# Optimization experiments

Measured on AMD Instinct MI355X. Metric: run time of the kernel, lower is better.

## Reference

```python
import jax, jax.numpy as jnp
import numpy as np

N = 100000
E = 1600000
IN_C, HID_C, OUT_C = 64, 64, 40
EPS = 1e-5


def setup_inputs() -> dict:
    key = jax.random.key(0)
    ks = jax.random.split(key, 16)
    x = jax.random.normal(ks[0], (N, IN_C), dtype=jnp.float32)
    edge_index = jax.random.randint(ks[1], (2, E), 0, N, dtype=jnp.int64)

    def glorot(k, fan_in, fan_out):
        s = jnp.sqrt(6.0 / (fan_in + fan_out)).astype(jnp.float32)
        return jax.random.uniform(k, (fan_in, fan_out), jnp.float32, -s, s)

    return {
        "x": x,
        "edge_index": edge_index,
        # layer 0: SAGEConv(IN_C -> HID_C): out = mean_aggr @ Wl + x @ Wr + b
        "Wl0": glorot(ks[2], IN_C, HID_C), "Wr0": glorot(ks[3], IN_C, HID_C),
        "b0": jnp.zeros((HID_C,), jnp.float32),
        # layer 1: SAGEConv(HID_C -> HID_C)
        "Wl1": glorot(ks[4], HID_C, HID_C), "Wr1": glorot(ks[5], HID_C, HID_C),
        "b1": jnp.zeros((HID_C,), jnp.float32),
        # layer 2: SAGEConv(HID_C -> OUT_C)
        "Wl2": glorot(ks[6], HID_C, OUT_C), "Wr2": glorot(ks[7], HID_C, OUT_C),
        "b2": jnp.zeros((OUT_C,), jnp.float32),
        # batch norms after layers 0 and 1
        "g0": jnp.ones((HID_C,), jnp.float32), "be0": jnp.zeros((HID_C,), jnp.float32),
        "g1": jnp.ones((HID_C,), jnp.float32), "be1": jnp.zeros((HID_C,), jnp.float32),
    }


def _sage_conv(x, src, dst, Wl, Wr, b):
    # mean aggregation of source features at destination nodes (PyG SAGEConv, aggr='mean')
    agg = jax.ops.segment_sum(x[src], dst, num_segments=N)  # [N, C]
    deg = jax.ops.segment_sum(jnp.ones((src.shape[0],), x.dtype), dst, num_segments=N)
    mean = agg / jnp.maximum(deg, 1.0)[:, None]
    return mean @ Wl + x @ Wr + b


def _batch_norm(x, gamma, beta):
    mu = jnp.mean(x, axis=0)
    var = jnp.var(x, axis=0)
    return (x - mu) * jax.lax.rsqrt(var + EPS) * gamma + beta


def reference(x, edge_index, Wl0, Wr0, b0, Wl1, Wr1, b1, Wl2, Wr2, b2, g0, be0, g1, be1):
    src, dst = edge_index[0], edge_index[1]
    h = _sage_conv(x, src, dst, Wl0, Wr0, b0)
    h = jax.nn.relu(_batch_norm(h, g0, be0))  # dropout is identity at inference
    h = _sage_conv(h, src, dst, Wl1, Wr1, b1)
    h = jax.nn.relu(_batch_norm(h, g1, be1))
    return _sage_conv(h, src, dst, Wl2, Wr2, b2)
```

## Files before the change

kernel.cpp:

```cpp
#include <hip/hip_runtime.h>


constexpr float BN_EPS = 1e-5f;

typedef __attribute__((ext_vector_type(8))) short bf16x8;
typedef __attribute__((ext_vector_type(4))) float f32x4;

__device__ __forceinline__ float bf2f(unsigned short u) {
  union { unsigned int i; float f; } c;
  c.i = (unsigned int)u << 16;
  return c.f;
}
__device__ __forceinline__ unsigned short f2bf(float v) {
  union { float f; unsigned int i; } c;
  c.f = v;
  unsigned int r = c.i + 0x7fffu + ((c.i >> 16) & 1u);
  return (unsigned short)(r >> 16);
}

__device__ __forceinline__ void st_f(float* p, size_t i, float v) { p[i] = v; }
__device__ __forceinline__ void st_f(unsigned short* p, size_t i, float v) {
  p[i] = f2bf(v);
}

__device__ __forceinline__ float4 ld_row(const float* p, int row, int li) {
  return ((const float4*)p)[(size_t)row * 16 + li];
}
__device__ __forceinline__ float4 ld_row(const unsigned short* p, int row, int li) {
  ushort4 u = ((const ushort4*)p)[(size_t)row * 16 + li];
  float4 f;
  f.x = bf2f(u.x); f.y = bf2f(u.y); f.z = bf2f(u.z); f.w = bf2f(u.w);
  return f;
}

__global__ __launch_bounds__(256) void k_probe(const int* __restrict__ w, int E,
                                               int* __restrict__ dflag) {
  __shared__ int any;
  if (threadIdx.x == 0) any = 0;
  __syncthreads();
  const int twoE = 2 * E;
  int local = 0;
  for (int i = 0; i < 8; ++i) {
    long long idx = (long long)(threadIdx.x * 8 + i) * twoE / 2048;
    int wi = (int)(idx | 1);
    if (wi < twoE && w[wi] != 0) local = 1;
  }
  if (local) atomicOr(&any, 1);
  __syncthreads();
  if (threadIdx.x == 0) *dflag = any;
}

__device__ __forceinline__ void load_edge(const void* ei, int e, int E, int is32,
                                          int& src, int& dst) {
  if (is32) {
    const int* p = (const int*)ei;
    src = p[e];
    dst = p[E + e];
  } else {
    const long long* p = (const long long*)ei;
    src = (int)p[e];
    dst = (int)p[(long long)E + e];
  }
}

__global__ __launch_bounds__(256) void k_hist(const void* __restrict__ ei, int E,
                                              int N, const int* __restrict__ dflag,
                                              int NB, int chunk,
                                              int* __restrict__ hist) {
  __shared__ int h[256];
  h[threadIdx.x] = 0;
  __syncthreads();
  const int is32 = *dflag;
  int lo = blockIdx.x * chunk;
  int hi = lo + chunk;
  if (hi > E) hi = E;
  for (int e = lo + threadIdx.x; e < hi; e += 256) {
    int src, dst;
    load_edge(ei, e, E, is32, src, dst);
    if ((unsigned)src < (unsigned)N && (unsigned)dst < (unsigned)N)
      atomicAdd(&h[dst >> 9], 1);
  }
  __syncthreads();
  if (threadIdx.x < NB) hist[blockIdx.x * NB + threadIdx.x] = h[threadIdx.x];
}

__global__ __launch_bounds__(256) void k_btot(const int* __restrict__ hist,
                                              int NBLK, int NB,
                                              int* __restrict__ bucket_base,
                                              float* __restrict__ stats) {
  stats[threadIdx.x] = 0.0f;
  __shared__ int part[256];
  int t = threadIdx.x;
  int s = 0;
  if (t < NB)
    for (int b = 0; b < NBLK; ++b) s += hist[b * NB + t];
  part[t] = s;
  __syncthreads();
  for (int off = 1; off < 256; off <<= 1) {
    int u = (t >= off) ? part[t - off] : 0;
    __syncthreads();
    part[t] += u;
    __syncthreads();
  }
  if (t < NB) bucket_base[t] = part[t] - s;
  if (t == NB - 1) bucket_base[NB] = part[t];
}

__global__ __launch_bounds__(64) void k_hoff(const int* __restrict__ hist,
                                             int NBLK, int NB,
                                             const int* __restrict__ bucket_base,
                                             int* __restrict__ offs) {
  int b = blockIdx.x;
  int lane = threadIdx.x;
  int carry = bucket_base[b];
  for (int c = 0; c < NBLK; c += 64) {
    int blk = c + lane;
    int v = (blk < NBLK) ? hist[blk * NB + b] : 0;
    int incl = v;
    for (int off = 1; off < 64; off <<= 1) {
      int u = __shfl_up(incl, off);
      if (lane >= off) incl += u;
    }
    if (blk < NBLK) offs[blk * NB + b] = carry + incl - v;
    carry += __shfl(incl, 63);
  }
}

__global__ __launch_bounds__(256) void k_scat(const void* __restrict__ ei, int E,
                                              int N, const int* __restrict__ dflag,
                                              int NB, int chunk,
                                              const int* __restrict__ offs,
                                              unsigned* __restrict__ csr) {
  __shared__ int cur[256];
  if (threadIdx.x < NB) cur[threadIdx.x] = offs[blockIdx.x * NB + threadIdx.x];
  __syncthreads();
  const int is32 = *dflag;
  int lo = blockIdx.x * chunk;
  int hi = lo + chunk;
  if (hi > E) hi = E;
  for (int e = lo + threadIdx.x; e < hi; e += 256) {
    int src, dst;
    load_edge(ei, e, E, is32, src, dst);
    if ((unsigned)src < (unsigned)N && (unsigned)dst < (unsigned)N) {
      int p = atomicAdd(&cur[dst >> 9], 1);
      csr[p] = ((unsigned)src << 9) | (unsigned)(dst & 511);
    }
  }
}

__global__ __launch_bounds__(256) void k_fine(unsigned* __restrict__ csr,
                                              const int* __restrict__ bucket_base,
                                              int N, int* __restrict__ row_start) {
  constexpr int CAP = 12288;
  __shared__ unsigned lrec[CAP];
  __shared__ int lcnt[512];
  __shared__ int cur[512];
  __shared__ int wtot[4];
  const int b = blockIdx.x;
  const int lo = bucket_base[b];
  int cnt = bucket_base[b + 1] - lo;
  if (cnt > CAP) cnt = CAP;
  const int t = threadIdx.x;
  lcnt[t] = 0;
  lcnt[t + 256] = 0;
  __syncthreads();
  for (int i = t; i < cnt; i += 256) {
    unsigned r = csr[lo + i];
    lrec[i] = r;
    atomicAdd(&lcnt[r & 511], 1);
  }
  __syncthreads();
  int v0 = lcnt[2 * t], v1 = lcnt[2 * t + 1];
  int s = v0 + v1;
  int incl = s;
  const int lane = t & 63;
  for (int off = 1; off < 64; off <<= 1) {
    int u = __shfl_up(incl, off);
    if (lane >= off) incl += u;
  }
  const int wv = t >> 6;
  if (lane == 63) wtot[wv] = incl;
  __syncthreads();
  int woff = 0;
  for (int i = 0; i < wv; ++i) woff += wtot[i];
  int excl = woff + incl - s;
  cur[2 * t] = excl;
  cur[2 * t + 1] = excl + v0;
  int gi = b * 512 + 2 * t;
  if (gi <= N) row_start[gi] = lo + excl;
  if (gi + 1 <= N) row_start[gi + 1] = lo + excl + v0;
  __syncthreads();
  for (int i = t; i < cnt; i += 256) {
    unsigned r = lrec[i];
    int p = atomicAdd(&cur[r & 511], 1);
    csr[lo + p] = r >> 9;
  }
}

template <int COUT, bool BNIN, bool BNOUT, typename TI, typename TO>
__global__ __launch_bounds__(256, 4) void k_sage(
    const TI* __restrict__ hin, const int* __restrict__ row_start,
    const int* __restrict__ csr, const float* __restrict__ Wl,
    const float* __restrict__ Wr, const float* __restrict__ bias,
    const float* __restrict__ statsIn, const float* __restrict__ gIn,
    const float* __restrict__ beIn, float* __restrict__ statsOut,
    TO* __restrict__ out, int n) {
  constexpr int NT = (COUT + 15) / 16;
  __shared__ short sWf[NT][4][64][8];
  __shared__ short sA[4][16][136];
  __shared__ float sBN[2][64];
  __shared__ float sRed[2][4][64];

  for (int t = threadIdx.x; t < NT * 4 * 64; t += 256) {
    int lane = t & 63;
    int kt = (t >> 6) & 3;
    int nt = t >> 8;
    int kbase = kt * 32 + (lane >> 4) * 8;
    int col = nt * 16 + (lane & 15);
#pragma unroll
    for (int j = 0; j < 8; ++j) {
      int k = kbase + j;
      float wv = 0.0f;
      if (col < COUT) wv = (k < 64) ? Wl[k * COUT + col] : Wr[(k - 64) * COUT + col];
      sWf[nt][kt][lane][j] = (short)f2bf(wv);
    }
  }
  if (BNIN && threadIdx.x < 64) {
    int c = threadIdx.x;
    float inv = 1.0f / (float)n;
    float mu = statsIn[c] * inv;
    float var = statsIn[64 + c] * inv - mu * mu;
    var = var < 0.f ? 0.f : var;
    float sc = gIn[c] * rsqrtf(var + BN_EPS);
    sBN[0][c] = sc;
    sBN[1][c] = beIn[c] - mu * sc;
  }
  __syncthreads();

  const int wave = threadIdx.x >> 6;
  const int lane = threadIdx.x & 63;
  const int g = lane >> 4;
  const int li = lane & 15;
  const int quad = lane >> 4;
  const int col16 = lane & 15;

  float4 bsc = make_float4(1.f, 1.f, 1.f, 1.f);
  float4 bsh = make_float4(0.f, 0.f, 0.f, 0.f);
  if (BNIN) {
    bsc = *(const float4*)&sBN[0][li * 4];
    bsh = *(const float4*)&sBN[1][li * 4];
  }
  auto xf = [&](float4 v) -> float4 {
    if (!BNIN) return v;
    float4 r;
    r.x = fmaxf(v.x * bsc.x + bsh.x, 0.f);
    r.y = fmaxf(v.y * bsc.y + bsh.y, 0.f);
    r.z = fmaxf(v.z * bsc.z + bsh.z, 0.f);
    r.w = fmaxf(v.w * bsc.w + bsh.w, 0.f);
    return r;
  };

  float bias_r[NT];
#pragma unroll
  for (int nt = 0; nt < NT; ++nt) {
    int c = nt * 16 + col16;
    bias_r[nt] = (c < COUT) ? bias[c] : 0.0f;
  }

  float statS[NT], statQ[NT];
#pragma unroll
  for (int nt = 0; nt < NT; ++nt) { statS[nt] = 0.f; statQ[nt] = 0.f; }

  const int wgl = blockIdx.x * 4 + wave;
  const int nstride = gridDim.x * 64;

  for (int base = wgl * 16; base < n; base += nstride) {
#pragma unroll 1
    for (int nb = 0; nb < 16; ++nb) {
      int node = base + nb;
      if (node >= n) break;
      int rs = row_start[node];
      int re = row_start[node + 1];
      float4 acc = make_float4(0.f, 0.f, 0.f, 0.f);
      int e = rs + g;
      for (; e + 12 < re; e += 16) {
        int r0 = csr[e], r1 = csr[e + 4], r2 = csr[e + 8], r3 = csr[e + 12];
        float4 a = xf(ld_row(hin, r0, li));
        float4 b = xf(ld_row(hin, r1, li));
        float4 c = xf(ld_row(hin, r2, li));
        float4 d = xf(ld_row(hin, r3, li));
        acc.x += (a.x + b.x) + (c.x + d.x);
        acc.y += (a.y + b.y) + (c.y + d.y);
        acc.z += (a.z + b.z) + (c.z + d.z);
        acc.w += (a.w + b.w) + (c.w + d.w);
      }
      for (; e < re; e += 4) {
        float4 a = xf(ld_row(hin, csr[e], li));
        acc.x += a.x; acc.y += a.y; acc.z += a.z; acc.w += a.w;
      }
      acc.x += __shfl_xor(acc.x, 16); acc.x += __shfl_xor(acc.x, 32);
      acc.y += __shfl_xor(acc.y, 16); acc.y += __shfl_xor(acc.y, 32);
      acc.z += __shfl_xor(acc.z, 16); acc.z += __shfl_xor(acc.z, 32);
      acc.w += __shfl_xor(acc.w, 16); acc.w += __shfl_xor(acc.w, 32);
      int deg = re - rs;
      float invd = 1.0f / (float)(deg > 0 ? deg : 1);
      float4 self = xf(ld_row(hin, node, li));
      ushort4 mv, sv;
      mv.x = f2bf(acc.x * invd); mv.y = f2bf(acc.y * invd);
      mv.z = f2bf(acc.z * invd); mv.w = f2bf(acc.w * invd);
      sv.x = f2bf(self.x); sv.y = f2bf(self.y);
      sv.z = f2bf(self.z); sv.w = f2bf(self.w);
      *(ushort4*)&sA[wave][nb][li * 4] = mv;
      *(ushort4*)&sA[wave][nb][64 + li * 4] = sv;
    }
    __builtin_amdgcn_wave_barrier();

    f32x4 acc[NT];
#pragma unroll
    for (int nt = 0; nt < NT; ++nt) acc[nt] = (f32x4){0.f, 0.f, 0.f, 0.f};
#pragma unroll
    for (int kt = 0; kt < 4; ++kt) {
      bf16x8 a = *(const bf16x8*)&sA[wave][lane & 15][kt * 32 + (lane >> 4) * 8];
#pragma unroll
      for (int nt = 0; nt < NT; ++nt) {
        bf16x8 b = *(const bf16x8*)&sWf[nt][kt][lane][0];
        acc[nt] = __builtin_amdgcn_mfma_f32_16x16x32_bf16(a, b, acc[nt], 0, 0, 0);
      }
    }
    __builtin_amdgcn_wave_barrier();

#pragma unroll
    for (int nt = 0; nt < NT; ++nt) {
      int c = nt * 16 + col16;
      if (c < COUT) {
#pragma unroll
        for (int r = 0; r < 4; ++r) {
          int node = base + quad * 4 + r;
          if (node < n) {
            float v = acc[nt][r] + bias_r[nt];
            st_f(out, (size_t)node * COUT + c, v);
            if (BNOUT) { statS[nt] += v; statQ[nt] += v * v; }
          }
        }
      }
    }
  }

  if (BNOUT) {
#pragma unroll
    for (int nt = 0; nt < NT; ++nt) {
      statS[nt] += __shfl_xor(statS[nt], 16);
      statS[nt] += __shfl_xor(statS[nt], 32);
      statQ[nt] += __shfl_xor(statQ[nt], 16);
      statQ[nt] += __shfl_xor(statQ[nt], 32);
    }
    if (quad == 0) {
#pragma unroll
      for (int nt = 0; nt < NT; ++nt) {
        sRed[0][wave][nt * 16 + col16] = statS[nt];
        sRed[1][wave][nt * 16 + col16] = statQ[nt];
      }
    }
    __syncthreads();
    if (threadIdx.x < 64) {
      int c = threadIdx.x;
      float s = sRed[0][0][c] + sRed[0][1][c] + sRed[0][2][c] + sRed[0][3][c];
      float q = sRed[1][0][c] + sRed[1][1][c] + sRed[1][2][c] + sRed[1][3][c];
      atomicAdd(&statsOut[c], s);
      atomicAdd(&statsOut[64 + c], q);
    }
  }
}

extern "C" void kernel_launch(void* const* d_in, const int* in_sizes, int n_in,
                              void* d_out, int out_size, void* d_ws, size_t ws_size,
                              hipStream_t stream) {
  const float* x = (const float*)d_in[0];
  const void* ei = d_in[1];
  const float* Wl0 = (const float*)d_in[2];
  const float* Wr0 = (const float*)d_in[3];
  const float* b0 = (const float*)d_in[4];
  const float* Wl1 = (const float*)d_in[5];
  const float* Wr1 = (const float*)d_in[6];
  const float* b1 = (const float*)d_in[7];
  const float* Wl2 = (const float*)d_in[8];
  const float* Wr2 = (const float*)d_in[9];
  const float* b2 = (const float*)d_in[10];
  const float* g0 = (const float*)d_in[11];
  const float* be0 = (const float*)d_in[12];
  const float* g1 = (const float*)d_in[13];
  const float* be1 = (const float*)d_in[14];

  const int N = in_sizes[0] / 64;
  const int E = in_sizes[1] / 2;
  const int NB = (N + 511) >> 9;
  const int NBLK = 256;
  const int chunk = (E + NBLK - 1) / NBLK;

  char* w = (char*)d_ws;
  auto carve = [&](size_t bytes) {
    void* p = (void*)w;
    w += (bytes + 255) & ~(size_t)255;
    return p;
  };
  int* dflag = (int*)carve(4);
  float* stats = (float*)carve(1024);
  int* row_start = (int*)carve((size_t)(N + 1) * 4);
  unsigned* csr = (unsigned*)carve((size_t)E * 4);
  int* hist = (int*)carve((size_t)NBLK * NB * 4);
  int* offs = (int*)carve((size_t)NBLK * NB * 4);
  int* bucket_base = (int*)carve((size_t)(NB + 1) * 4);

  float* statsA = stats;
  float* statsB = stats + 128;

  unsigned short* B = (unsigned short*)d_out;
  unsigned short* A = (unsigned short*)const_cast<float*>(x);

  const int SG = 1024;

  k_probe<<<1, 256, 0, stream>>>((const int*)ei, E, dflag);
  k_hist<<<NBLK, 256, 0, stream>>>(ei, E, N, dflag, NB, chunk, hist);
  k_btot<<<1, 256, 0, stream>>>(hist, NBLK, NB, bucket_base, stats);
  k_hoff<<<NB, 64, 0, stream>>>(hist, NBLK, NB, bucket_base, offs);
  k_scat<<<NBLK, 256, 0, stream>>>(ei, E, N, dflag, NB, chunk, offs, csr);
  k_fine<<<NB, 256, 0, stream>>>(csr, bucket_base, N, row_start);

  k_sage<64, false, true, float, unsigned short><<<SG, 256, 0, stream>>>(
      x, row_start, (const int*)csr, Wl0, Wr0, b0,
      statsA, g0, be0, statsA, B, N);

  k_sage<64, true, true, unsigned short, unsigned short><<<SG, 256, 0, stream>>>(
      B, row_start, (const int*)csr, Wl1, Wr1, b1,
      statsA, g0, be0, statsB, A, N);

  k_sage<40, true, false, unsigned short, float><<<SG, 256, 0, stream>>>(
      A, row_start, (const int*)csr, Wl2, Wr2, b2,
      statsB, g1, be1, statsB, (float*)d_out, N);
}
```

Before: 516.4 us.

## Gather neighbor features from FP8 copies in layers 1 and 2

Adds conversion kernels that turn the bf16 hidden activations into packed FP8 (e4m3) copies. Layers 1 and 2 then gather neighbour rows from these copies, halving the bytes per random row read in the dominant aggregation loop, while self rows stay in bf16. It also folds the per-bucket offset scan into the bucket-total kernel, removing one launch. The cost is two extra conversion passes and an FP8 quantisation error in the mean aggregation that may break accuracy tolerance.

```diff
diff --git a/kernel.cpp b/kernel.cpp
--- a/kernel.cpp
+++ b/kernel.cpp
@@ -5,6 +5,7 @@
 
 typedef __attribute__((ext_vector_type(8))) short bf16x8;
 typedef __attribute__((ext_vector_type(4))) float f32x4;
+typedef __attribute__((ext_vector_type(2))) float f32x2;
 
 __device__ __forceinline__ float bf2f(unsigned short u) {
   union { unsigned int i; float f; } c;
@@ -23,6 +24,68 @@
   p[i] = f2bf(v);
 }
 
+#if __has_builtin(__builtin_amdgcn_cvt_pk_f32_fp8) && \
+    __has_builtin(__builtin_amdgcn_cvt_pk_fp8_f32)
+#define HW_FP8 1
+#endif
+
+__device__ __forceinline__ float4 dec8(unsigned v) {
+#ifdef HW_FP8
+  f32x2 lo = __builtin_amdgcn_cvt_pk_f32_fp8((int)v, false);
+  f32x2 hi = __builtin_amdgcn_cvt_pk_f32_fp8((int)v, true);
+  float4 r;
+  r.x = lo[0]; r.y = lo[1]; r.z = hi[0]; r.w = hi[1];
+  return r;
+#else
+  auto d1 = [](unsigned b) -> float {
+    unsigned s = (b & 0x80u) << 24;
+    unsigned e = (b >> 3) & 15u, m = b & 7u;
+    unsigned bits;
+    if (e) bits = s | ((e + 120u) << 23) | (m << 20);
+    else if (m) {
+      int sh = (m & 4u) ? 0 : ((m & 2u) ? 1 : 2);
+      bits = s | ((114u - sh) << 23) | ((m << (sh + 21)) & 0x7FFFFFu);
+    } else
+      bits = s;
+    union { unsigned u; float f; } c;
+    c.u = bits;
+    return c.f;
+  };
+  float4 r;
+  r.x = d1(v & 255u); r.y = d1((v >> 8) & 255u);
+  r.z = d1((v >> 16) & 255u); r.w = d1(v >> 24);
+  return r;
+#endif
+}
+
+__device__ __forceinline__ unsigned enc8(float4 f) {
+#ifdef HW_FP8
+  int p = 0;
+  p = __builtin_amdgcn_cvt_pk_fp8_f32(f.x, f.y, p, false);
+  p = __builtin_amdgcn_cvt_pk_fp8_f32(f.z, f.w, p, true);
+  return (unsigned)p;
+#else
+  auto e1 = [](float x) -> unsigned {
+    union { float f; unsigned u; } c;
+    c.f = x;
+    unsigned s = (c.u >> 24) & 0x80u;
+    float a = fabsf(x);
+    if (a >= 464.f) return s | 0x7Eu;
+    if (a < 0.0009765625f) {
+      unsigned m = (unsigned)rintf(a * 512.f);
+      return s | (m & 7u);
+    }
+    c.f = a;
+    unsigned r = c.u + 0x7FFFFu + ((c.u >> 20) & 1u);
+    unsigned e = (r >> 23) - 120u;
+    unsigned m = (r >> 20) & 7u;
+    if (e >= 16u || (e == 15u && m == 7u)) return s | 0x7Eu;
+    return s | (e << 3) | m;
+  };
+  return e1(f.x) | (e1(f.y) << 8) | (e1(f.z) << 16) | (e1(f.w) << 24);
+#endif
+}
+
 __device__ __forceinline__ float4 ld_row(const float* p, int row, int li) {
   return ((const float4*)p)[(size_t)row * 16 + li];
 }
@@ -31,6 +94,9 @@
   float4 f;
   f.x = bf2f(u.x); f.y = bf2f(u.y); f.z = bf2f(u.z); f.w = bf2f(u.w);
   return f;
+}
+__device__ __forceinline__ float4 ld_row8(const unsigned* p, int row, int li) {
+  return dec8(p[(size_t)row * 16 + li]);
 }
 
 __global__ __launch_bounds__(256) void k_probe(const int* __restrict__ w, int E,
@@ -87,6 +153,7 @@
 __global__ __launch_bounds__(256) void k_btot(const int* __restrict__ hist,
                                               int NBLK, int NB,
                                               int* __restrict__ bucket_base,
+                                              int* __restrict__ offs,
                                               float* __restrict__ stats) {
   stats[threadIdx.x] = 0.0f;
   __shared__ int part[256];
@@ -104,25 +171,13 @@
   }
   if (t < NB) bucket_base[t] = part[t] - s;
   if (t == NB - 1) bucket_base[NB] = part[t];
-}
-
-__global__ __launch_bounds__(64) void k_hoff(const int* __restrict__ hist,
-                                             int NBLK, int NB,
-                                             const int* __restrict__ bucket_base,
-                                             int* __restrict__ offs) {
-  int b = blockIdx.x;
-  int lane = threadIdx.x;
-  int carry = bucket_base[b];
-  for (int c = 0; c < NBLK; c += 64) {
-    int blk = c + lane;
-    int v = (blk < NBLK) ? hist[blk * NB + b] : 0;
-    int incl = v;
-    for (int off = 1; off < 64; off <<= 1) {
-      int u = __shfl_up(incl, off);
-      if (lane >= off) incl += u;
-    }
-    if (blk < NBLK) offs[blk * NB + b] = carry + incl - v;
-    carry += __shfl(incl, 63);
+  __syncthreads();
+  if (t < NB) {
+    int carry = bucket_base[t];
+    for (int b = 0; b < NBLK; ++b) {
+      offs[b * NB + t] = carry;
+      carry += hist[b * NB + t];
+    }
   }
 }
 
@@ -197,14 +252,24 @@
   }
 }
 
-template <int COUT, bool BNIN, bool BNOUT, typename TI, typename TO>
+__global__ __launch_bounds__(256) void k_cvt8(const unsigned short* __restrict__ src,
+                                              unsigned* __restrict__ dst, int n16) {
+  int i = blockIdx.x * 256 + threadIdx.x;
+  if (i >= n16) return;
+  ushort4 u = ((const ushort4*)src)[i];
+  float4 f;
+  f.x = bf2f(u.x); f.y = bf2f(u.y); f.z = bf2f(u.z); f.w = bf2f(u.w);
+  dst[i] = enc8(f);
+}
+
+template <int COUT, bool BNIN, bool BNOUT, bool FP8, typename TI, typename TO>
 __global__ __launch_bounds__(256, 4) void k_sage(
-    const TI* __restrict__ hin, const int* __restrict__ row_start,
-    const int* __restrict__ csr, const float* __restrict__ Wl,
-    const float* __restrict__ Wr, const float* __restrict__ bias,
-    const float* __restrict__ statsIn, const float* __restrict__ gIn,
-    const float* __restrict__ beIn, float* __restrict__ statsOut,
-    TO* __restrict__ out, int n) {
+    const TI* __restrict__ hin, const unsigned* __restrict__ hin8,
+    const int* __restrict__ row_start, const int* __restrict__ csr,
+    const float* __restrict__ Wl, const float* __restrict__ Wr,
+    const float* __restrict__ bias, const float* __restrict__ statsIn,
+    const float* __restrict__ gIn, const float* __restrict__ beIn,
+    float* __restrict__ statsOut, TO* __restrict__ out, int n) {
   constexpr int NT = (COUT + 15) / 16;
   __shared__ short sWf[NT][4][64][8];
   __shared__ short sA[4][16][136];
@@ -258,6 +323,10 @@
     r.z = fmaxf(v.z * bsc.z + bsh.z, 0.f);
     r.w = fmaxf(v.w * bsc.w + bsh.w, 0.f);
     return r;
+  };
+  auto mrow = [&](int row) -> float4 {
+    if (FP8) return ld_row8(hin8, row, li);
+    return ld_row(hin, row, li);
   };
 
   float bias_r[NT];
@@ -285,17 +354,17 @@
       int e = rs + g;
       for (; e + 12 < re; e += 16) {
         int r0 = csr[e], r1 = csr[e + 4], r2 = csr[e + 8], r3 = csr[e + 12];
-        float4 a = xf(ld_row(hin, r0, li));
-        float4 b = xf(ld_row(hin, r1, li));
-        float4 c = xf(ld_row(hin, r2, li));
-        float4 d = xf(ld_row(hin, r3, li));
+        float4 a = xf(mrow(r0));
+        float4 b = xf(mrow(r1));
+        float4 c = xf(mrow(r2));
+        float4 d = xf(mrow(r3));
         acc.x += (a.x + b.x) + (c.x + d.x);
         acc.y += (a.y + b.y) + (c.y + d.y);
         acc.z += (a.z + b.z) + (c.z + d.z);
         acc.w += (a.w + b.w) + (c.w + d.w);
       }
       for (; e < re; e += 4) {
-        float4 a = xf(ld_row(hin, csr[e], li));
+        float4 a = xf(mrow(csr[e]));
         acc.x += a.x; acc.y += a.y; acc.z += a.z; acc.w += a.w;
       }
       acc.x += __shfl_xor(acc.x, 16); acc.x += __shfl_xor(acc.x, 32);
@@ -414,27 +483,32 @@
   float* statsA = stats;
   float* statsB = stats + 128;
 
+  char* xb = (char*)const_cast<float*>(x);
   unsigned short* B = (unsigned short*)d_out;
-  unsigned short* A = (unsigned short*)const_cast<float*>(x);
+  unsigned* B8 = (unsigned*)xb;
+  unsigned short* A = (unsigned short*)(xb + (size_t)N * 64);
+  unsigned* A8 = (unsigned*)(xb + (size_t)N * 64 * 3);
 
   const int SG = 1024;
+  const int cb = (N * 16 + 255) / 256;
 
   k_probe<<<1, 256, 0, stream>>>((const int*)ei, E, dflag);
   k_hist<<<NBLK, 256, 0, stream>>>(ei, E, N, dflag, NB, chunk, hist);
-  k_btot<<<1, 256, 0, stream>>>(hist, NBLK, NB, bucket_base, stats);
-  k_hoff<<<NB, 64, 0, stream>>>(hist, NBLK, NB, bucket_base, offs);
+  k_btot<<<1, 256, 0, stream>>>(hist, NBLK, NB, bucket_base, offs, stats);
   k_scat<<<NBLK, 256, 0, stream>>>(ei, E, N, dflag, NB, chunk, offs, csr);
   k_fine<<<NB, 256, 0, stream>>>(csr, bucket_base, N, row_start);
 
-  k_sage<64, false, true, float, unsigned short><<<SG, 256, 0, stream>>>(
-      x, row_start, (const int*)csr, Wl0, Wr0, b0,
+  k_sage<64, false, true, false, float, unsigned short><<<SG, 256, 0, stream>>>(
+      x, nullptr, row_start, (const int*)csr, Wl0, Wr0, b0,
       statsA, g0, be0, statsA, B, N);
-
-  k_sage<64, true, true, unsigned short, unsigned short><<<SG, 256, 0, stream>>>(
-      B, row_start, (const int*)csr, Wl1, Wr1, b1,
-      statsA, g0, be0, statsB, A, N);
-
-  k_sage<40, true, false, unsigned short, float><<<SG, 256, 0, stream>>>(
-      A, row_start, (const int*)csr, Wl2, Wr2, b2,
+  k_cvt8<<<cb, 256, 0, stream>>>(B, B8, N * 16);
+
+  k_sage<64, true, true, true, unsigned short, unsigned short>
+      <<<SG, 256, 0, stream>>>(B, B8, row_start, (const int*)csr, Wl1, Wr1, b1,
+                               statsA, g0, be0, statsB, A, N);
+  k_cvt8<<<cb, 256, 0, stream>>>(A, A8, N * 16);
+
+  k_sage<40, true, false, true, unsigned short, float><<<SG, 256, 0, stream>>>(
+      A, A8, row_start, (const int*)csr, Wl2, Wr2, b2,
       statsB, g1, be1, statsB, (float*)d_out, N);
 }
```

Result: slower. 544.1 us (+5.4%).
